# Kernel optimization log

Measured on AMD Instinct MI355X. Metric: run time of the kernel, lower is better.

## Reference

```python
import jax, jax.numpy as jnp
import numpy as np

N = 100000      # nodes
E = 3200000     # edges
D_IN, D_H, D_OUT = 128, 64, 32


def _lin(key, fan_in, fan_out):
    kw, kb = jax.random.split(key)
    s = 1.0 / np.sqrt(fan_in)
    W = jax.random.uniform(kw, (fan_in, fan_out), jnp.float32, -s, s)
    b = jax.random.uniform(kb, (fan_out,), jnp.float32, -s, s)
    return W, b


def setup_inputs() -> dict:
    key = jax.random.key(0)
    ks = jax.random.split(key, 8)
    x = jax.random.normal(ks[0], (N, D_IN), jnp.float32)
    edge_index = jax.random.randint(ks[1], (2, E), 0, N, dtype=jnp.int32).astype(jnp.int64)
    W1, b1 = _lin(ks[2], D_IN, D_H)      # GCNConv(128, 64)
    W2, b2 = _lin(ks[3], D_H, D_OUT)     # GCNConv(64, 32)
    rW1, rb1 = _lin(ks[4], D_OUT, D_H)   # reconstruction MLP
    rW2, rb2 = _lin(ks[5], D_H, D_IN)
    sW1, sb1 = _lin(ks[6], D_OUT, D_H // 2)  # anomaly scorer MLP
    sW2, sb2 = _lin(ks[7], D_H // 2, 1)
    return {"x": x, "edge_index": edge_index,
            "W1": W1, "b1": b1, "W2": W2, "b2": b2,
            "rW1": rW1, "rb1": rb1, "rW2": rW2, "rb2": rb2,
            "sW1": sW1, "sb1": sb1, "sW2": sW2, "sb2": sb2}


def gcn_conv(h, W, b, src, dst, deg_inv_sqrt):
    # GCNConv with added self-loops and symmetric normalization.
    hw = h @ W                                   # [N, out]
    norm = deg_inv_sqrt[src] * deg_inv_sqrt[dst] # [E]
    agg = jax.ops.segment_sum(hw[src] * norm[:, None], dst, num_segments=N)
    agg = agg + hw * (deg_inv_sqrt * deg_inv_sqrt)[:, None]  # self-loop term
    return agg + b


def reference(x, edge_index, W1, b1, W2, b2, rW1, rb1, rW2, rb2, sW1, sb1, sW2, sb2):
    src, dst = edge_index[0], edge_index[1]
    # degree with self-loops (in-degree on target, as in PyG gcn_norm)
    deg = jnp.zeros((N,), x.dtype).at[dst].add(1.0) + 1.0
    dis = jax.lax.rsqrt(deg)
    h = gcn_conv(x, W1, b1, src, dst, dis)
    h = jax.nn.relu(h)                           # relu+dropout(eval=no-op) between convs
    h = gcn_conv(h, W2, b2, src, dst, dis)       # [N, 32]
    x_rec = jax.nn.relu(h @ rW1 + rb1) @ rW2 + rb2           # [N, 128]
    score = jax.nn.sigmoid(jax.nn.relu(h @ sW1 + sb1) @ sW2 + sb2)  # [N, 1]
    return h, x_rec, score
```

## Files before the change

### kernel.cpp

```cpp
#include <hip/hip_runtime.h>
#include <hip/hip_bf16.h>
#include <math.h>


__global__ void k_detect(const unsigned int* __restrict__ w, int npairs,
                         int* __restrict__ meta) {
  __shared__ int any;
  if (threadIdx.x == 0) any = 0;
  __syncthreads();
  int local = 0;
  for (int i = threadIdx.x; i < npairs; i += blockDim.x)
    local |= (w[2 * i + 1] != 0u);
  if (local) atomicOr(&any, 1);
  __syncthreads();
  if (threadIdx.x == 0) meta[0] = any ? 0 : 1;
}

__global__ __launch_bounds__(256) void k_binhist(const void* __restrict__ ei,
                                                 int E, int CS, int B, int shift,
                                                 const int* __restrict__ meta,
                                                 int* __restrict__ hist, int C) {
  __shared__ int lh[256];
  int c = blockIdx.x;
  for (int i = threadIdx.x; i < B; i += 256) lh[i] = 0;
  __syncthreads();
  int e0 = c * CS, e1 = min(E, e0 + CS);
  bool is64 = meta[0] != 0;
  for (int e = e0 + threadIdx.x; e < e1; e += 256) {
    int d = is64 ? (int)((const long long*)ei)[(long)E + e]
                 : ((const int*)ei)[(long)E + e];
    atomicAdd(&lh[d >> shift], 1);
  }
  __syncthreads();
  for (int b = threadIdx.x; b < B; b += 256) hist[(long)b * C + c] = lh[b];
}

__global__ __launch_bounds__(256) void k_binscatter(const void* __restrict__ ei,
                                                    int E, int CS, int B, int shift,
                                                    int SB,
                                                    const int* __restrict__ meta,
                                                    const int* __restrict__ scan,
                                                    int C, unsigned* __restrict__ pairs) {
  __shared__ int cur[256];
  int c = blockIdx.x;
  for (int b = threadIdx.x; b < B; b += 256) cur[b] = scan[(long)b * C + c];
  __syncthreads();
  int e0 = c * CS, e1 = min(E, e0 + CS);
  bool is64 = meta[0] != 0;
  unsigned spb1 = (1u << shift) - 1u;
  for (int e = e0 + threadIdx.x; e < e1; e += 256) {
    int s, d;
    if (is64) {
      const long long* p = (const long long*)ei;
      s = (int)p[e]; d = (int)p[(long)E + e];
    } else {
      const int* p = (const int*)ei;
      s = p[e]; d = p[(long)E + e];
    }
    int pos = atomicAdd(&cur[d >> shift], 1);
    pairs[pos] = (((unsigned)d & spb1) << SB) | (unsigned)s;
  }
}

#define BB_CAP 16896
__global__ __launch_bounds__(256) void k_bucketbuild(const unsigned* __restrict__ pairs,
                                                     const int* __restrict__ scan,
                                                     int C, int shift, int SB, int N,
                                                     int* __restrict__ cnt,
                                                     float* __restrict__ dis,
                                                     int* __restrict__ rs,
                                                     int* __restrict__ csr) {
  __shared__ unsigned buf[BB_CAP];
  __shared__ unsigned buf2[BB_CAP];
  __shared__ int h[1024];
  __shared__ int sm[256];
  __shared__ int sh[512];
  int bin = blockIdx.x;
  int base = bin << shift;
  int nn = min(N - base, 1 << shift);
  int t = threadIdx.x;
  unsigned smask = (1u << SB) - 1u;
  int p0 = scan[(long)bin * C];
  int p1 = scan[(long)(bin + 1) * C];
  int ne = p1 - p0;
  bool srt = (ne <= BB_CAP);

  if (srt)
    for (int i = t; i < ne; i += 256) buf[i] = pairs[p0 + i];
  for (int i = t; i < 1024; i += 256) h[i] = 0;
  __syncthreads();

  for (int i = t; i < ne; i += 256)
    atomicAdd(&h[(srt ? buf[i] : pairs[p0 + i]) >> SB], 1);
  __syncthreads();

  int v0 = h[4 * t], v1 = h[4 * t + 1], v2 = h[4 * t + 2], v3 = h[4 * t + 3];
  int s = v0 + v1 + v2 + v3;
  sm[t] = s;
  __syncthreads();
  for (int off = 1; off < 256; off <<= 1) {
    int x = (t >= off) ? sm[t - off] : 0;
    __syncthreads();
    sm[t] += x;
    __syncthreads();
  }
  int run = p0 + sm[t] - s;
  int r0 = run, r1 = run + v0, r2 = r1 + v1, r3 = r2 + v2;
  h[4 * t] = r0; h[4 * t + 1] = r1; h[4 * t + 2] = r2; h[4 * t + 3] = r3;
  if (4 * t + 0 < nn) { cnt[base + 4*t+0] = v0; dis[base + 4*t+0] = rsqrtf((float)v0 + 1.f); rs[base + 4*t+0] = r0; }
  if (4 * t + 1 < nn) { cnt[base + 4*t+1] = v1; dis[base + 4*t+1] = rsqrtf((float)v1 + 1.f); rs[base + 4*t+1] = r1; }
  if (4 * t + 2 < nn) { cnt[base + 4*t+2] = v2; dis[base + 4*t+2] = rsqrtf((float)v2 + 1.f); rs[base + 4*t+2] = r2; }
  if (4 * t + 3 < nn) { cnt[base + 4*t+3] = v3; dis[base + 4*t+3] = rsqrtf((float)v3 + 1.f); rs[base + 4*t+3] = r3; }
  __syncthreads();

  if (srt) {
    for (int i = t; i < 512; i += 256) sh[i] = 0;
    __syncthreads();
    for (int i = t; i < ne; i += 256)
      atomicAdd(&sh[(buf[i] & smask) >> 8], 1);
    __syncthreads();
    int a0 = sh[2 * t], a1 = sh[2 * t + 1];
    int ss = a0 + a1;
    sm[t] = ss;
    __syncthreads();
    for (int off = 1; off < 256; off <<= 1) {
      int x = (t >= off) ? sm[t - off] : 0;
      __syncthreads();
      sm[t] += x;
      __syncthreads();
    }
    int rn = sm[t] - ss;
    sh[2 * t] = rn; sh[2 * t + 1] = rn + a0;
    __syncthreads();
    for (int i = t; i < ne; i += 256) {
      unsigned p = buf[i];
      int pos = atomicAdd(&sh[(p & smask) >> 8], 1);
      buf2[pos] = p;
    }
    __syncthreads();
    for (int i = t; i < ne; i += 256) {
      unsigned p = buf2[i];
      int pos = atomicAdd(&h[p >> SB], 1);
      csr[pos] = (int)(p & smask);
    }
  } else {
    for (int i = p0 + t; i < p1; i += 256) {
      unsigned p = pairs[i];
      int pos = atomicAdd(&h[p >> SB], 1);
      csr[pos] = (int)(p & smask);
    }
  }
}

__global__ __launch_bounds__(1024) void k_scan1(const int* __restrict__ cnt,
                                                int* __restrict__ bsums, int n) {
  __shared__ int sm[1024];
  int t = threadIdx.x;
  long i = (long)blockIdx.x * 1024 + t;
  sm[t] = (i < n) ? cnt[i] : 0;
  __syncthreads();
  for (int s = 512; s > 0; s >>= 1) {
    if (t < s) sm[t] += sm[t + s];
    __syncthreads();
  }
  if (t == 0) bsums[blockIdx.x] = sm[0];
}

__global__ void k_scan2(int* __restrict__ bsums, int nb) {
  __shared__ int sm[128];
  int t = threadIdx.x;
  int v = (t < nb) ? bsums[t] : 0;
  sm[t] = v;
  __syncthreads();
  for (int off = 1; off < 128; off <<= 1) {
    int x = (t >= off) ? sm[t - off] : 0;
    __syncthreads();
    sm[t] += x;
    __syncthreads();
  }
  if (t < nb) bsums[t] = sm[t] - v;
}

__global__ __launch_bounds__(1024) void k_scan3s(const int* __restrict__ in,
                                                 const int* __restrict__ bsums,
                                                 int* __restrict__ out, int n,
                                                 int sentinel) {
  __shared__ int sm[1024];
  int t = threadIdx.x;
  long i = (long)blockIdx.x * 1024 + t;
  int v = (i < n) ? in[i] : 0;
  sm[t] = v;
  __syncthreads();
  for (int off = 1; off < 1024; off <<= 1) {
    int x = (t >= off) ? sm[t - off] : 0;
    __syncthreads();
    sm[t] += x;
    __syncthreads();
  }
  int excl = sm[t] - v + bsums[blockIdx.x];
  if (i < n) out[i] = excl;
  if (sentinel && i == n - 1) out[n] = excl + v;
}

__device__ __forceinline__ float bfu(unsigned short u) {
  return __uint_as_float((unsigned)u << 16);
}
__device__ __forceinline__ float bf_lo(unsigned u) {
  return __uint_as_float(u << 16);
}
__device__ __forceinline__ float bf_hi(unsigned u) {
  return __uint_as_float(u & 0xffff0000u);
}
__device__ __forceinline__ unsigned pack_bf2(float lo, float hi) {
  __hip_bfloat16 a = __float2bfloat16(lo), b = __float2bfloat16(hi);
  return (unsigned)*(unsigned short*)&a | ((unsigned)*(unsigned short*)&b << 16);
}

template <int K, int M, bool BIAS, int ACT, bool ABF16, bool OBF16>
__global__ __launch_bounds__(256) void k_gemm(const void* __restrict__ Av,
                                              const float* __restrict__ W,
                                              const float* __restrict__ bias,
                                              void* __restrict__ Cout, int nrows) {
  constexpr int CP = 4;
  constexpr int TPR = M / CP;
  constexpr int RG = 256 / TPR;
  constexpr int RP = 4;
  constexpr int RT = RG * RP;
  __shared__ __align__(16) float sW[K * M];
  __shared__ __align__(16) float sB[BIAS ? M : 4];

  for (int i = threadIdx.x; i < K * M / 4; i += 256)
    ((float4*)sW)[i] = ((const float4*)W)[i];
  if (BIAS)
    for (int i = threadIdx.x; i < M; i += 256) sB[i] = bias[i];
  __syncthreads();

  const int cg = threadIdx.x % TPR;
  const int rg = threadIdx.x / TPR;
  const long row0 = (long)blockIdx.x * RT + rg;

  const float4* Apf[RP];
  const ushort4* Apb[RP];
  bool valid[RP];
#pragma unroll
  for (int r = 0; r < RP; ++r) {
    long row = row0 + (long)r * RG;
    valid[r] = (row < nrows);
    long rr = valid[r] ? row : 0;
    if (ABF16) Apb[r] = (const ushort4*)((const unsigned short*)Av + rr * K);
    else       Apf[r] = (const float4*)((const float*)Av + rr * K);
  }

  auto loadA = [&](int r, int k4) -> float4 {
    if (!valid[r]) return make_float4(0.f, 0.f, 0.f, 0.f);
    if (ABF16) {
      ushort4 q = Apb[r][k4];
      return make_float4(bfu(q.x), bfu(q.y), bfu(q.z), bfu(q.w));
    }
    return Apf[r][k4];
  };

  float acc[RP][CP] = {};
  float4 a[RP];
#pragma unroll
  for (int r = 0; r < RP; ++r) a[r] = loadA(r, 0);

#pragma unroll 1
  for (int k0 = 0; k0 < K - 4; k0 += 4) {
    float4 an[RP];
#pragma unroll
    for (int r = 0; r < RP; ++r) an[r] = loadA(r, k0 / 4 + 1);
#pragma unroll
    for (int j = 0; j < 4; ++j) {
      float4 w = ((const float4*)(sW + (k0 + j) * M))[cg];
#pragma unroll
      for (int r = 0; r < RP; ++r) {
        float av = (j == 0) ? a[r].x : (j == 1) ? a[r].y : (j == 2) ? a[r].z : a[r].w;
        acc[r][0] += av * w.x;
        acc[r][1] += av * w.y;
        acc[r][2] += av * w.z;
        acc[r][3] += av * w.w;
      }
    }
#pragma unroll
    for (int r = 0; r < RP; ++r) a[r] = an[r];
  }
  {
    const int k0 = K - 4;
#pragma unroll
    for (int j = 0; j < 4; ++j) {
      float4 w = ((const float4*)(sW + (k0 + j) * M))[cg];
#pragma unroll
      for (int r = 0; r < RP; ++r) {
        float av = (j == 0) ? a[r].x : (j == 1) ? a[r].y : (j == 2) ? a[r].z : a[r].w;
        acc[r][0] += av * w.x;
        acc[r][1] += av * w.y;
        acc[r][2] += av * w.z;
        acc[r][3] += av * w.w;
      }
    }
  }

#pragma unroll
  for (int r = 0; r < RP; ++r) {
    long row = row0 + (long)r * RG;
    if (row >= nrows) continue;
    float4 o = make_float4(acc[r][0], acc[r][1], acc[r][2], acc[r][3]);
    if (BIAS) {
      float4 bb = ((const float4*)sB)[cg];
      o.x += bb.x; o.y += bb.y; o.z += bb.z; o.w += bb.w;
    }
    if (ACT == 1) {
      o.x = fmaxf(o.x, 0.f); o.y = fmaxf(o.y, 0.f);
      o.z = fmaxf(o.z, 0.f); o.w = fmaxf(o.w, 0.f);
    }
    if (OBF16) {
      uint2 pk;
      pk.x = pack_bf2(o.x, o.y);
      pk.y = pack_bf2(o.z, o.w);
      ((uint2*)((__hip_bfloat16*)Cout + row * M))[cg] = pk;
    } else {
      ((float4*)((float*)Cout + row * M))[cg] = o;
    }
  }
}

__global__ __launch_bounds__(256) void k_agg64p(const uint2* __restrict__ hw,
                                                const int* __restrict__ csr,
                                                const int* __restrict__ rs,
                                                const int* __restrict__ cnt,
                                                const float* __restrict__ dis,
                                                const float* __restrict__ b,
                                                uint2* __restrict__ out, int n) {
  unsigned node = blockIdx.x * 16u + (threadIdx.x >> 4);
  if (node >= (unsigned)n) return;
  unsigned f4 = threadIdx.x & 15;
  float dsn = dis[node];
  uint2 su = hw[node * 16u + f4];
  float d2 = dsn * dsn;
  float a0 = bf_lo(su.x) * d2, a1 = bf_hi(su.x) * d2;
  float a2 = bf_lo(su.y) * d2, a3 = bf_hi(su.y) * d2;
  int start = rs[node], deg = cnt[node];
  int e = 0;
  for (; e + 7 < deg; e += 8) {
    unsigned s0 = (unsigned)csr[start + e];
    unsigned s1 = (unsigned)csr[start + e + 1];
    unsigned s2 = (unsigned)csr[start + e + 2];
    unsigned s3 = (unsigned)csr[start + e + 3];
    unsigned s4 = (unsigned)csr[start + e + 4];
    unsigned s5 = (unsigned)csr[start + e + 5];
    unsigned s6 = (unsigned)csr[start + e + 6];
    unsigned s7 = (unsigned)csr[start + e + 7];
    float w0 = dis[s0] * dsn, w1 = dis[s1] * dsn;
    float w2 = dis[s2] * dsn, w3 = dis[s3] * dsn;
    float w4 = dis[s4] * dsn, w5 = dis[s5] * dsn;
    float w6 = dis[s6] * dsn, w7 = dis[s7] * dsn;
    uint2 u0 = hw[s0 * 16u + f4];
    uint2 u1 = hw[s1 * 16u + f4];
    uint2 u2 = hw[s2 * 16u + f4];
    uint2 u3 = hw[s3 * 16u + f4];
    uint2 u4 = hw[s4 * 16u + f4];
    uint2 u5 = hw[s5 * 16u + f4];
    uint2 u6 = hw[s6 * 16u + f4];
    uint2 u7 = hw[s7 * 16u + f4];
    a0 += bf_lo(u0.x) * w0 + bf_lo(u1.x) * w1 + bf_lo(u2.x) * w2 + bf_lo(u3.x) * w3
        + bf_lo(u4.x) * w4 + bf_lo(u5.x) * w5 + bf_lo(u6.x) * w6 + bf_lo(u7.x) * w7;
    a1 += bf_hi(u0.x) * w0 + bf_hi(u1.x) * w1 + bf_hi(u2.x) * w2 + bf_hi(u3.x) * w3
        + bf_hi(u4.x) * w4 + bf_hi(u5.x) * w5 + bf_hi(u6.x) * w6 + bf_hi(u7.x) * w7;
    a2 += bf_lo(u0.y) * w0 + bf_lo(u1.y) * w1 + bf_lo(u2.y) * w2 + bf_lo(u3.y) * w3
        + bf_lo(u4.y) * w4 + bf_lo(u5.y) * w5 + bf_lo(u6.y) * w6 + bf_lo(u7.y) * w7;
    a3 += bf_hi(u0.y) * w0 + bf_hi(u1.y) * w1 + bf_hi(u2.y) * w2 + bf_hi(u3.y) * w3
        + bf_hi(u4.y) * w4 + bf_hi(u5.y) * w5 + bf_hi(u6.y) * w6 + bf_hi(u7.y) * w7;
  }
  for (; e < deg; ++e) {
    unsigned s0 = (unsigned)csr[start + e];
    float w0 = dis[s0] * dsn;
    uint2 u0 = hw[s0 * 16u + f4];
    a0 += bf_lo(u0.x) * w0;
    a1 += bf_hi(u0.x) * w0;
    a2 += bf_lo(u0.y) * w0;
    a3 += bf_hi(u0.y) * w0;
  }
  float4 bb = ((const float4*)b)[f4];
  uint2 pk;
  pk.x = pack_bf2(fmaxf(a0 + bb.x, 0.f), fmaxf(a1 + bb.y, 0.f));
  pk.y = pack_bf2(fmaxf(a2 + bb.z, 0.f), fmaxf(a3 + bb.w, 0.f));
  out[node * 16u + f4] = pk;
}

__global__ __launch_bounds__(256) void k_agg32p(const uint2* __restrict__ hw,
                                                const int* __restrict__ csr,
                                                const int* __restrict__ rs,
                                                const int* __restrict__ cnt,
                                                const float* __restrict__ dis,
                                                const float* __restrict__ b,
                                                float* __restrict__ out, int n) {
  unsigned node = blockIdx.x * 32u + (threadIdx.x >> 3);
  if (node >= (unsigned)n) return;
  unsigned f4 = threadIdx.x & 7;
  float dsn = dis[node];
  uint2 su = hw[node * 8u + f4];
  float d2 = dsn * dsn;
  float a0 = bf_lo(su.x) * d2, a1 = bf_hi(su.x) * d2;
  float a2 = bf_lo(su.y) * d2, a3 = bf_hi(su.y) * d2;
  int start = rs[node], deg = cnt[node];
  int e = 0;
  for (; e + 7 < deg; e += 8) {
    unsigned s0 = (unsigned)csr[start + e];
    unsigned s1 = (unsigned)csr[start + e + 1];
    unsigned s2 = (unsigned)csr[start + e + 2];
    unsigned s3 = (unsigned)csr[start + e + 3];
    unsigned s4 = (unsigned)csr[start + e + 4];
    unsigned s5 = (unsigned)csr[start + e + 5];
    unsigned s6 = (unsigned)csr[start + e + 6];
    unsigned s7 = (unsigned)csr[start + e + 7];
    float w0 = dis[s0] * dsn, w1 = dis[s1] * dsn;
    float w2 = dis[s2] * dsn, w3 = dis[s3] * dsn;
    float w4 = dis[s4] * dsn, w5 = dis[s5] * dsn;
    float w6 = dis[s6] * dsn, w7 = dis[s7] * dsn;
    uint2 u0 = hw[s0 * 8u + f4];
    uint2 u1 = hw[s1 * 8u + f4];
    uint2 u2 = hw[s2 * 8u + f4];
    uint2 u3 = hw[s3 * 8u + f4];
    uint2 u4 = hw[s4 * 8u + f4];
    uint2 u5 = hw[s5 * 8u + f4];
    uint2 u6 = hw[s6 * 8u + f4];
    uint2 u7 = hw[s7 * 8u + f4];
    a0 += bf_lo(u0.x) * w0 + bf_lo(u1.x) * w1 + bf_lo(u2.x) * w2 + bf_lo(u3.x) * w3
        + bf_lo(u4.x) * w4 + bf_lo(u5.x) * w5 + bf_lo(u6.x) * w6 + bf_lo(u7.x) * w7;
    a1 += bf_hi(u0.x) * w0 + bf_hi(u1.x) * w1 + bf_hi(u2.x) * w2 + bf_hi(u3.x) * w3
        + bf_hi(u4.x) * w4 + bf_hi(u5.x) * w5 + bf_hi(u6.x) * w6 + bf_hi(u7.x) * w7;
    a2 += bf_lo(u0.y) * w0 + bf_lo(u1.y) * w1 + bf_lo(u2.y) * w2 + bf_lo(u3.y) * w3
        + bf_lo(u4.y) * w4 + bf_lo(u5.y) * w5 + bf_lo(u6.y) * w6 + bf_lo(u7.y) * w7;
    a3 += bf_hi(u0.y) * w0 + bf_hi(u1.y) * w1 + bf_hi(u2.y) * w2 + bf_hi(u3.y) * w3
        + bf_hi(u4.y) * w4 + bf_hi(u5.y) * w5 + bf_hi(u6.y) * w6 + bf_hi(u7.y) * w7;
  }
  for (; e < deg; ++e) {
    unsigned s0 = (unsigned)csr[start + e];
    float w0 = dis[s0] * dsn;
    uint2 u0 = hw[s0 * 8u + f4];
    a0 += bf_lo(u0.x) * w0;
    a1 += bf_hi(u0.x) * w0;
    a2 += bf_lo(u0.y) * w0;
    a3 += bf_hi(u0.y) * w0;
  }
  float4 bb = ((const float4*)b)[f4];
  ((float4*)(out + node * 32u))[f4] =
      make_float4(a0 + bb.x, a1 + bb.y, a2 + bb.z, a3 + bb.w);
}

__global__ __launch_bounds__(256) void k_tail(const float* __restrict__ h,
                                              const float* __restrict__ rW1,
                                              const float* __restrict__ rb1,
                                              const float* __restrict__ rW2,
                                              const float* __restrict__ rb2,
                                              const float* __restrict__ sW1,
                                              const float* __restrict__ sb1,
                                              const float* __restrict__ sW2,
                                              const float* __restrict__ sb2,
                                              float* __restrict__ x_rec,
                                              float* __restrict__ score, int n) {
  __shared__ __align__(16) float sRW1[32 * 64];
  __shared__ __align__(16) float sRW2[64 * 128];
  __shared__ __align__(16) float sSW1[32 * 32];
  __shared__ __align__(16) float sRB1[64];
  __shared__ __align__(16) float sRB2[128];
  __shared__ __align__(16) float sSB1[32];
  __shared__ __align__(16) float sSW2[32];
  __shared__ float sH[64 * 33];
  __shared__ float sT[64 * 65];
  __shared__ float sS[64 * 33];
  int t = threadIdx.x;
  for (int i = t; i < 32 * 64 / 4; i += 256) ((float4*)sRW1)[i] = ((const float4*)rW1)[i];
  for (int i = t; i < 64 * 128 / 4; i += 256) ((float4*)sRW2)[i] = ((const float4*)rW2)[i];
  for (int i = t; i < 32 * 32 / 4; i += 256) ((float4*)sSW1)[i] = ((const float4*)sW1)[i];
  if (t < 64) sRB1[t] = rb1[t];
  else if (t < 192) sRB2[t - 64] = rb2[t - 64];
  else if (t < 224) sSB1[t - 192] = sb1[t - 192];
  else sSW2[t - 224] = sW2[t - 224];

  long base = (long)blockIdx.x * 64;
  int nn = (int)min(64L, (long)n - base);
  if (nn < 0) nn = 0;
  for (int i = t; i < 64 * 8; i += 256) {
    int node = i >> 3, q = i & 7;
    float4 v = (node < nn) ? ((const float4*)(h + (base + node) * 32))[q]
                           : make_float4(0.f, 0.f, 0.f, 0.f);
    sH[node * 33 + 4 * q]     = v.x;
    sH[node * 33 + 4 * q + 1] = v.y;
    sH[node * 33 + 4 * q + 2] = v.z;
    sH[node * 33 + 4 * q + 3] = v.w;
  }
  __syncthreads();

  {
    int cg = t & 15, rg = t >> 4;
    float acc[4][4] = {};
    for (int k = 0; k < 32; ++k) {
      float4 w = ((const float4*)(sRW1 + k * 64))[cg];
      float a0 = sH[rg * 33 + k];
      float a1 = sH[(rg + 16) * 33 + k];
      float a2 = sH[(rg + 32) * 33 + k];
      float a3 = sH[(rg + 48) * 33 + k];
      acc[0][0] += a0 * w.x; acc[0][1] += a0 * w.y; acc[0][2] += a0 * w.z; acc[0][3] += a0 * w.w;
      acc[1][0] += a1 * w.x; acc[1][1] += a1 * w.y; acc[1][2] += a1 * w.z; acc[1][3] += a1 * w.w;
      acc[2][0] += a2 * w.x; acc[2][1] += a2 * w.y; acc[2][2] += a2 * w.z; acc[2][3] += a2 * w.w;
      acc[3][0] += a3 * w.x; acc[3][1] += a3 * w.y; acc[3][2] += a3 * w.z; acc[3][3] += a3 * w.w;
    }
    float4 bb = ((const float4*)sRB1)[cg];
#pragma unroll
    for (int m = 0; m < 4; ++m) {
      int row = rg + 16 * m;
      sT[row * 65 + 4 * cg]     = fmaxf(acc[m][0] + bb.x, 0.f);
      sT[row * 65 + 4 * cg + 1] = fmaxf(acc[m][1] + bb.y, 0.f);
      sT[row * 65 + 4 * cg + 2] = fmaxf(acc[m][2] + bb.z, 0.f);
      sT[row * 65 + 4 * cg + 3] = fmaxf(acc[m][3] + bb.w, 0.f);
    }
  }
  {
    int cg = t & 7, rg = t >> 3;
    float acc[2][4] = {};
    for (int k = 0; k < 32; ++k) {
      float4 w = ((const float4*)(sSW1 + k * 32))[cg];
      float a0 = sH[rg * 33 + k];
      float a1 = sH[(rg + 32) * 33 + k];
      acc[0][0] += a0 * w.x; acc[0][1] += a0 * w.y; acc[0][2] += a0 * w.z; acc[0][3] += a0 * w.w;
      acc[1][0] += a1 * w.x; acc[1][1] += a1 * w.y; acc[1][2] += a1 * w.z; acc[1][3] += a1 * w.w;
    }
    float4 bb = ((const float4*)sSB1)[cg];
#pragma unroll
    for (int m = 0; m < 2; ++m) {
      int row = rg + 32 * m;
      sS[row * 33 + 4 * cg]     = fmaxf(acc[m][0] + bb.x, 0.f);
      sS[row * 33 + 4 * cg + 1] = fmaxf(acc[m][1] + bb.y, 0.f);
      sS[row * 33 + 4 * cg + 2] = fmaxf(acc[m][2] + bb.z, 0.f);
      sS[row * 33 + 4 * cg + 3] = fmaxf(acc[m][3] + bb.w, 0.f);
    }
  }
  __syncthreads();

  {
    int cg = t & 31, rg = t >> 5;
    float acc[8][4] = {};
    for (int k = 0; k < 64; ++k) {
      float4 w = ((const float4*)(sRW2 + k * 128))[cg];
#pragma unroll
      for (int m = 0; m < 8; ++m) {
        float a = sT[(rg + 8 * m) * 65 + k];
        acc[m][0] += a * w.x; acc[m][1] += a * w.y;
        acc[m][2] += a * w.z; acc[m][3] += a * w.w;
      }
    }
    float4 bb = ((const float4*)sRB2)[cg];
#pragma unroll
    for (int m = 0; m < 8; ++m) {
      int row = rg + 8 * m;
      if (row < nn) {
        float4 o = make_float4(acc[m][0] + bb.x, acc[m][1] + bb.y,
                               acc[m][2] + bb.z, acc[m][3] + bb.w);
        ((float4*)(x_rec + (base + row) * 128))[cg] = o;
      }
    }
  }
  if (t < nn) {
    float acc = 0.f;
    for (int j = 0; j < 32; ++j) acc += sS[t * 33 + j] * sSW2[j];
    score[base + t] = 1.0f / (1.0f + expf(-(acc + sb2[0])));
  }
}

extern "C" void kernel_launch(void* const* d_in, const int* in_sizes, int n_in,
                              void* d_out, int out_size, void* d_ws, size_t ws_size,
                              hipStream_t stream) {
  const float* x   = (const float*)d_in[0];
  const void*  ei  = d_in[1];
  const float* W1  = (const float*)d_in[2];
  const float* b1  = (const float*)d_in[3];
  const float* W2  = (const float*)d_in[4];
  const float* b2  = (const float*)d_in[5];
  const float* rW1 = (const float*)d_in[6];
  const float* rb1 = (const float*)d_in[7];
  const float* rW2 = (const float*)d_in[8];
  const float* rb2 = (const float*)d_in[9];
  const float* sW1 = (const float*)d_in[10];
  const float* sb1 = (const float*)d_in[11];
  const float* sW2 = (const float*)d_in[12];
  const float* sb2 = (const float*)d_in[13];

  const int N = in_sizes[0] / 128;
  const int E = in_sizes[1] / 2;

  int shift = 9;
  while ((((long)N + (1L << shift) - 1) >> shift) > 256) ++shift;
  const int SB = 32 - shift;
  const int B = (int)(((long)N + (1L << shift) - 1) >> shift);
  const int C = 512;
  const int CS = (E + C - 1) / C;
  const int L = B * C;

  char* w = (char*)d_ws;
  auto alloc = [&](size_t bytes) {
    char* p = w;
    w += (bytes + 255) & ~(size_t)255;
    return p;
  };
  int*   meta   = (int*)alloc(64);
  int*   cnt    = (int*)alloc((size_t)N * 4);
  int*   rs     = (int*)alloc((size_t)N * 4);
  float* dis    = (float*)alloc((size_t)N * 4);
  int*   bsumsL = (int*)alloc(1024);
  int*   bscan  = (int*)alloc(((size_t)L + 1) * 4);
  int*   csr    = (int*)alloc((size_t)E * 4);
  unsigned* pairs = (unsigned*)alloc((size_t)E * 4);
  uint2* hw1 = (uint2*)alloc((size_t)N * 64 * 2);
  uint2* h1  = (uint2*)alloc((size_t)N * 64 * 2);
  uint2* hw2 = (uint2*)alloc((size_t)N * 32 * 2);

  float* h_out = (float*)d_out;
  float* x_rec = h_out + (long)N * 32;
  float* score = x_rec + (long)N * 128;

  k_detect<<<1, 256, 0, stream>>>((const unsigned int*)ei, E < 4096 ? E : 4096, meta);
  k_binhist<<<C, 256, 0, stream>>>(ei, E, CS, B, shift, meta, bscan, C);
  int nbL = (L + 1023) / 1024;
  k_scan1<<<nbL, 1024, 0, stream>>>(bscan, bsumsL, L);
  k_scan2<<<1, 128, 0, stream>>>(bsumsL, nbL);
  k_scan3s<<<nbL, 1024, 0, stream>>>(bscan, bsumsL, bscan, L, 1);
  k_binscatter<<<C, 256, 0, stream>>>(ei, E, CS, B, shift, SB, meta, bscan, C, pairs);
  k_bucketbuild<<<B, 256, 0, stream>>>(pairs, bscan, C, shift, SB, N, cnt, dis, rs, csr);

  k_gemm<128, 64, false, 0, false, true><<<(N + 63) / 64, 256, 0, stream>>>(x, W1, nullptr, hw1, N);
  k_agg64p<<<(N + 15) / 16, 256, 0, stream>>>(hw1, csr, rs, cnt, dis, b1, h1, N);

  k_gemm<64, 32, false, 0, true, true><<<(N + 127) / 128, 256, 0, stream>>>(h1, W2, nullptr, hw2, N);
  k_agg32p<<<(N + 31) / 32, 256, 0, stream>>>(hw2, csr, rs, cnt, dis, b2, h_out, N);

  k_tail<<<(N + 63) / 64, 256, 0, stream>>>(h_out, rW1, rb1, rW2, rb2,
                                            sW1, sb1, sW2, sb2, x_rec, score, N);
}
```

Baseline: 298.2 us.

## Fuse second GEMM into first aggregation and fold dtype detection into edge kernels

The first-layer aggregation kernel now keeps its ReLU'd output in shared memory and multiplies it by W2 directly, writing hw2 in bf16. This removes the separate h1 buffer write/read and one GEMM launch. The int32/int64 edge-index detection kernel is dropped; each block of binhist and binscatter instead scans the first 4096 pairs itself, saving a launch but repeating that small read in every block. The aggregation kernel gains shared memory and a barrier, which may lower occupancy.

```diff
diff --git a/kernel.cpp b/kernel.cpp
--- a/kernel.cpp
+++ b/kernel.cpp
@@ -3,52 +3,58 @@
 #include <math.h>
 
 
-__global__ void k_detect(const unsigned int* __restrict__ w, int npairs,
-                         int* __restrict__ meta) {
-  __shared__ int any;
-  if (threadIdx.x == 0) any = 0;
-  __syncthreads();
-  int local = 0;
-  for (int i = threadIdx.x; i < npairs; i += blockDim.x)
-    local |= (w[2 * i + 1] != 0u);
-  if (local) atomicOr(&any, 1);
-  __syncthreads();
-  if (threadIdx.x == 0) meta[0] = any ? 0 : 1;
-}
-
 __global__ __launch_bounds__(256) void k_binhist(const void* __restrict__ ei,
                                                  int E, int CS, int B, int shift,
-                                                 const int* __restrict__ meta,
+                                                 int ndet,
                                                  int* __restrict__ hist, int C) {
   __shared__ int lh[256];
+  __shared__ int s32;
+  int t = threadIdx.x;
+  if (t == 0) s32 = 0;
+  for (int i = t; i < B; i += 256) lh[i] = 0;
+  __syncthreads();
+  {
+    const unsigned* w = (const unsigned*)ei;
+    int local = 0;
+    for (int i = t; i < ndet; i += 256) local |= (w[2 * i + 1] != 0u);
+    if (local) atomicOr(&s32, 1);
+  }
+  __syncthreads();
+  bool is64 = (s32 == 0);
   int c = blockIdx.x;
-  for (int i = threadIdx.x; i < B; i += 256) lh[i] = 0;
-  __syncthreads();
   int e0 = c * CS, e1 = min(E, e0 + CS);
-  bool is64 = meta[0] != 0;
-  for (int e = e0 + threadIdx.x; e < e1; e += 256) {
+  for (int e = e0 + t; e < e1; e += 256) {
     int d = is64 ? (int)((const long long*)ei)[(long)E + e]
                  : ((const int*)ei)[(long)E + e];
     atomicAdd(&lh[d >> shift], 1);
   }
   __syncthreads();
-  for (int b = threadIdx.x; b < B; b += 256) hist[(long)b * C + c] = lh[b];
+  for (int b = t; b < B; b += 256) hist[(long)b * C + c] = lh[b];
 }
 
 __global__ __launch_bounds__(256) void k_binscatter(const void* __restrict__ ei,
                                                     int E, int CS, int B, int shift,
-                                                    int SB,
-                                                    const int* __restrict__ meta,
+                                                    int SB, int ndet,
                                                     const int* __restrict__ scan,
                                                     int C, unsigned* __restrict__ pairs) {
   __shared__ int cur[256];
+  __shared__ int s32;
+  int t = threadIdx.x;
+  if (t == 0) s32 = 0;
   int c = blockIdx.x;
-  for (int b = threadIdx.x; b < B; b += 256) cur[b] = scan[(long)b * C + c];
-  __syncthreads();
+  for (int b = t; b < B; b += 256) cur[b] = scan[(long)b * C + c];
+  __syncthreads();
+  {
+    const unsigned* w = (const unsigned*)ei;
+    int local = 0;
+    for (int i = t; i < ndet; i += 256) local |= (w[2 * i + 1] != 0u);
+    if (local) atomicOr(&s32, 1);
+  }
+  __syncthreads();
+  bool is64 = (s32 == 0);
   int e0 = c * CS, e1 = min(E, e0 + CS);
-  bool is64 = meta[0] != 0;
   unsigned spb1 = (1u << shift) - 1u;
-  for (int e = e0 + threadIdx.x; e < e1; e += 256) {
+  for (int e = e0 + t; e < e1; e += 256) {
     int s, d;
     if (is64) {
       const long long* p = (const long long*)ei;
@@ -325,67 +331,92 @@
   }
 }
 
-__global__ __launch_bounds__(256) void k_agg64p(const uint2* __restrict__ hw,
+__global__ __launch_bounds__(256) void k_agg64g(const uint2* __restrict__ hw,
                                                 const int* __restrict__ csr,
                                                 const int* __restrict__ rs,
                                                 const int* __restrict__ cnt,
                                                 const float* __restrict__ dis,
                                                 const float* __restrict__ b,
-                                                uint2* __restrict__ out, int n) {
-  unsigned node = blockIdx.x * 16u + (threadIdx.x >> 4);
-  if (node >= (unsigned)n) return;
-  unsigned f4 = threadIdx.x & 15;
-  float dsn = dis[node];
-  uint2 su = hw[node * 16u + f4];
-  float d2 = dsn * dsn;
-  float a0 = bf_lo(su.x) * d2, a1 = bf_hi(su.x) * d2;
-  float a2 = bf_lo(su.y) * d2, a3 = bf_hi(su.y) * d2;
-  int start = rs[node], deg = cnt[node];
-  int e = 0;
-  for (; e + 7 < deg; e += 8) {
-    unsigned s0 = (unsigned)csr[start + e];
-    unsigned s1 = (unsigned)csr[start + e + 1];
-    unsigned s2 = (unsigned)csr[start + e + 2];
-    unsigned s3 = (unsigned)csr[start + e + 3];
-    unsigned s4 = (unsigned)csr[start + e + 4];
-    unsigned s5 = (unsigned)csr[start + e + 5];
-    unsigned s6 = (unsigned)csr[start + e + 6];
-    unsigned s7 = (unsigned)csr[start + e + 7];
-    float w0 = dis[s0] * dsn, w1 = dis[s1] * dsn;
-    float w2 = dis[s2] * dsn, w3 = dis[s3] * dsn;
-    float w4 = dis[s4] * dsn, w5 = dis[s5] * dsn;
-    float w6 = dis[s6] * dsn, w7 = dis[s7] * dsn;
-    uint2 u0 = hw[s0 * 16u + f4];
-    uint2 u1 = hw[s1 * 16u + f4];
-    uint2 u2 = hw[s2 * 16u + f4];
-    uint2 u3 = hw[s3 * 16u + f4];
-    uint2 u4 = hw[s4 * 16u + f4];
-    uint2 u5 = hw[s5 * 16u + f4];
-    uint2 u6 = hw[s6 * 16u + f4];
-    uint2 u7 = hw[s7 * 16u + f4];
-    a0 += bf_lo(u0.x) * w0 + bf_lo(u1.x) * w1 + bf_lo(u2.x) * w2 + bf_lo(u3.x) * w3
-        + bf_lo(u4.x) * w4 + bf_lo(u5.x) * w5 + bf_lo(u6.x) * w6 + bf_lo(u7.x) * w7;
-    a1 += bf_hi(u0.x) * w0 + bf_hi(u1.x) * w1 + bf_hi(u2.x) * w2 + bf_hi(u3.x) * w3
-        + bf_hi(u4.x) * w4 + bf_hi(u5.x) * w5 + bf_hi(u6.x) * w6 + bf_hi(u7.x) * w7;
-    a2 += bf_lo(u0.y) * w0 + bf_lo(u1.y) * w1 + bf_lo(u2.y) * w2 + bf_lo(u3.y) * w3
-        + bf_lo(u4.y) * w4 + bf_lo(u5.y) * w5 + bf_lo(u6.y) * w6 + bf_lo(u7.y) * w7;
-    a3 += bf_hi(u0.y) * w0 + bf_hi(u1.y) * w1 + bf_hi(u2.y) * w2 + bf_hi(u3.y) * w3
-        + bf_hi(u4.y) * w4 + bf_hi(u5.y) * w5 + bf_hi(u6.y) * w6 + bf_hi(u7.y) * w7;
-  }
-  for (; e < deg; ++e) {
-    unsigned s0 = (unsigned)csr[start + e];
-    float w0 = dis[s0] * dsn;
-    uint2 u0 = hw[s0 * 16u + f4];
-    a0 += bf_lo(u0.x) * w0;
-    a1 += bf_hi(u0.x) * w0;
-    a2 += bf_lo(u0.y) * w0;
-    a3 += bf_hi(u0.y) * w0;
-  }
-  float4 bb = ((const float4*)b)[f4];
-  uint2 pk;
-  pk.x = pack_bf2(fmaxf(a0 + bb.x, 0.f), fmaxf(a1 + bb.y, 0.f));
-  pk.y = pack_bf2(fmaxf(a2 + bb.z, 0.f), fmaxf(a3 + bb.w, 0.f));
-  out[node * 16u + f4] = pk;
+                                                const float* __restrict__ W2,
+                                                unsigned* __restrict__ hw2,
+                                                int n) {
+  __shared__ __align__(16) float sW2[64 * 32];
+  __shared__ __align__(16) float sH[16][68];
+  int t = threadIdx.x;
+  for (int i = t; i < 64 * 32 / 4; i += 256)
+    ((float4*)sW2)[i] = ((const float4*)W2)[i];
+
+  unsigned nd = t >> 4;
+  unsigned node = blockIdx.x * 16u + nd;
+  unsigned f4 = t & 15;
+  bool ok = (node < (unsigned)n);
+  float o0 = 0.f, o1 = 0.f, o2 = 0.f, o3 = 0.f;
+  if (ok) {
+    float dsn = dis[node];
+    uint2 su = hw[node * 16u + f4];
+    float d2 = dsn * dsn;
+    float a0 = bf_lo(su.x) * d2, a1 = bf_hi(su.x) * d2;
+    float a2 = bf_lo(su.y) * d2, a3 = bf_hi(su.y) * d2;
+    int start = rs[node], deg = cnt[node];
+    int e = 0;
+    for (; e + 7 < deg; e += 8) {
+      unsigned s0 = (unsigned)csr[start + e];
+      unsigned s1 = (unsigned)csr[start + e + 1];
+      unsigned s2 = (unsigned)csr[start + e + 2];
+      unsigned s3 = (unsigned)csr[start + e + 3];
+      unsigned s4 = (unsigned)csr[start + e + 4];
+      unsigned s5 = (unsigned)csr[start + e + 5];
+      unsigned s6 = (unsigned)csr[start + e + 6];
+      unsigned s7 = (unsigned)csr[start + e + 7];
+      float w0 = dis[s0] * dsn, w1 = dis[s1] * dsn;
+      float w2 = dis[s2] * dsn, w3 = dis[s3] * dsn;
+      float w4 = dis[s4] * dsn, w5 = dis[s5] * dsn;
+      float w6 = dis[s6] * dsn, w7 = dis[s7] * dsn;
+      uint2 u0 = hw[s0 * 16u + f4];
+      uint2 u1 = hw[s1 * 16u + f4];
+      uint2 u2 = hw[s2 * 16u + f4];
+      uint2 u3 = hw[s3 * 16u + f4];
+      uint2 u4 = hw[s4 * 16u + f4];
+      uint2 u5 = hw[s5 * 16u + f4];
+      uint2 u6 = hw[s6 * 16u + f4];
+      uint2 u7 = hw[s7 * 16u + f4];
+      a0 += bf_lo(u0.x) * w0 + bf_lo(u1.x) * w1 + bf_lo(u2.x) * w2 + bf_lo(u3.x) * w3
+          + bf_lo(u4.x) * w4 + bf_lo(u5.x) * w5 + bf_lo(u6.x) * w6 + bf_lo(u7.x) * w7;
+      a1 += bf_hi(u0.x) * w0 + bf_hi(u1.x) * w1 + bf_hi(u2.x) * w2 + bf_hi(u3.x) * w3
+          + bf_hi(u4.x) * w4 + bf_hi(u5.x) * w5 + bf_hi(u6.x) * w6 + bf_hi(u7.x) * w7;
+      a2 += bf_lo(u0.y) * w0 + bf_lo(u1.y) * w1 + bf_lo(u2.y) * w2 + bf_lo(u3.y) * w3
+          + bf_lo(u4.y) * w4 + bf_lo(u5.y) * w5 + bf_lo(u6.y) * w6 + bf_lo(u7.y) * w7;
+      a3 += bf_hi(u0.y) * w0 + bf_hi(u1.y) * w1 + bf_hi(u2.y) * w2 + bf_hi(u3.y) * w3
+          + bf_hi(u4.y) * w4 + bf_hi(u5.y) * w5 + bf_hi(u6.y) * w6 + bf_hi(u7.y) * w7;
+    }
+    for (; e < deg; ++e) {
+      unsigned s0 = (unsigned)csr[start + e];
+      float w0 = dis[s0] * dsn;
+      uint2 u0 = hw[s0 * 16u + f4];
+      a0 += bf_lo(u0.x) * w0;
+      a1 += bf_hi(u0.x) * w0;
+      a2 += bf_lo(u0.y) * w0;
+      a3 += bf_hi(u0.y) * w0;
+    }
+    float4 bb = ((const float4*)b)[f4];
+    o0 = fmaxf(a0 + bb.x, 0.f);
+    o1 = fmaxf(a1 + bb.y, 0.f);
+    o2 = fmaxf(a2 + bb.z, 0.f);
+    o3 = fmaxf(a3 + bb.w, 0.f);
+  }
+  ((float4*)&sH[nd][4 * f4])[0] = make_float4(o0, o1, o2, o3);
+  __syncthreads();
+  if (ok) {
+    float acc0 = 0.f, acc1 = 0.f;
+#pragma unroll 8
+    for (int k = 0; k < 64; ++k) {
+      float hv = sH[nd][k];
+      float2 w = *(const float2*)(sW2 + k * 32 + 2 * f4);
+      acc0 += hv * w.x;
+      acc1 += hv * w.y;
+    }
+    hw2[node * 16u + f4] = pack_bf2(acc0, acc1);
+  }
 }
 
 __global__ __launch_bounds__(256) void k_agg32p(const uint2* __restrict__ hw,
@@ -589,6 +620,7 @@
 
   const int N = in_sizes[0] / 128;
   const int E = in_sizes[1] / 2;
+  const int ndet = E < 4096 ? E : 4096;
 
   int shift = 9;
   while ((((long)N + (1L << shift) - 1) >> shift) > 256) ++shift;
@@ -604,7 +636,6 @@
     w += (bytes + 255) & ~(size_t)255;
     return p;
   };
-  int*   meta   = (int*)alloc(64);
   int*   cnt    = (int*)alloc((size_t)N * 4);
   int*   rs     = (int*)alloc((size_t)N * 4);
   float* dis    = (float*)alloc((size_t)N * 4);
@@ -613,27 +644,24 @@
   int*   csr    = (int*)alloc((size_t)E * 4);
   unsigned* pairs = (unsigned*)alloc((size_t)E * 4);
   uint2* hw1 = (uint2*)alloc((size_t)N * 64 * 2);
-  uint2* h1  = (uint2*)alloc((size_t)N * 64 * 2);
-  uint2* hw2 = (uint2*)alloc((size_t)N * 32 * 2);
+  unsigned* hw2 = (unsigned*)alloc((size_t)N * 32 * 2);
 
   float* h_out = (float*)d_out;
   float* x_rec = h_out + (long)N * 32;
   float* score = x_rec + (long)N * 128;
 
-  k_detect<<<1, 256, 0, stream>>>((const unsigned int*)ei, E < 4096 ? E : 4096, meta);
-  k_binhist<<<C, 256, 0, stream>>>(ei, E, CS, B, shift, meta, bscan, C);
+  k_binhist<<<C, 256, 0, stream>>>(ei, E, CS, B, shift, ndet, bscan, C);
   int nbL = (L + 1023) / 1024;
   k_scan1<<<nbL, 1024, 0, stream>>>(bscan, bsumsL, L);
   k_scan2<<<1, 128, 0, stream>>>(bsumsL, nbL);
   k_scan3s<<<nbL, 1024, 0, stream>>>(bscan, bsumsL, bscan, L, 1);
-  k_binscatter<<<C, 256, 0, stream>>>(ei, E, CS, B, shift, SB, meta, bscan, C, pairs);
+  k_binscatter<<<C, 256, 0, stream>>>(ei, E, CS, B, shift, SB, ndet, bscan, C, pairs);
   k_bucketbuild<<<B, 256, 0, stream>>>(pairs, bscan, C, shift, SB, N, cnt, dis, rs, csr);
 
   k_gemm<128, 64, false, 0, false, true><<<(N + 63) / 64, 256, 0, stream>>>(x, W1, nullptr, hw1, N);
-  k_agg64p<<<(N + 15) / 16, 256, 0, stream>>>(hw1, csr, rs, cnt, dis, b1, h1, N);
-
-  k_gemm<64, 32, false, 0, true, true><<<(N + 127) / 128, 256, 0, stream>>>(h1, W2, nullptr, hw2, N);
-  k_agg32p<<<(N + 31) / 32, 256, 0, stream>>>(hw2, csr, rs, cnt, dis, b2, h_out, N);
+  k_agg64g<<<(N + 15) / 16, 256, 0, stream>>>(hw1, csr, rs, cnt, dis, b1, W2, hw2, N);
+
+  k_agg32p<<<(N + 31) / 32, 256, 0, stream>>>((const uint2*)hw2, csr, rs, cnt, dis, b2, h_out, N);
 
   k_tail<<<(N + 63) / 64, 256, 0, stream>>>(h_out, rW1, rb1, rW2, rb2,
                                             sW1, sb1, sW2, sb2, x_rec, score, N);
```

Measured after the change: 281.1 us. -5.7%, faster.
